# Performance work log

Hardware: AMD Instinct MI355X
Metric: run time of the kernel (lower is better)

Reference implementation:

```python
import math
import jax, jax.numpy as jnp
import numpy as np

B, S, D, H = 4, 1024, 512, 8
DH = D // H  # 64
SQRT_DIM = math.sqrt(D)


def _relative_shift(pos_score):
    # pos_score: [B, H, S, S]
    b, h, s1, s2 = pos_score.shape
    zeros = jnp.zeros((b, h, s1, 1), dtype=pos_score.dtype)
    padded = jnp.concatenate([zeros, pos_score], axis=-1)      # [B,H,S,S+1]
    padded = padded.reshape(b, h, s2 + 1, s1)                  # [B,H,S+1,S]
    return padded[:, :, 1:].reshape(b, h, s1, s2)


def setup_inputs() -> dict:
    key = jax.random.key(0)
    ks = jax.random.split(key, 14)
    std = 0.02
    inp = {
        "query": jax.random.normal(ks[0], (B, S, D), jnp.float32),
        "key": jax.random.normal(ks[1], (B, S, D), jnp.float32),
        "value": jax.random.normal(ks[2], (B, S, D), jnp.float32),
        "pos_embedding": jax.random.normal(ks[3], (B, S, D), jnp.float32),
        # projection weights stored [in, out] so y = x @ W + b
        "Wq": jax.random.normal(ks[4], (D, D), jnp.float32) * std,
        "bq": jnp.zeros((D,), jnp.float32),
        "Wk": jax.random.normal(ks[5], (D, D), jnp.float32) * std,
        "bk": jnp.zeros((D,), jnp.float32),
        "Wv": jax.random.normal(ks[6], (D, D), jnp.float32) * std,
        "bv": jnp.zeros((D,), jnp.float32),
        "Wp": jax.random.normal(ks[7], (D, D), jnp.float32) * std,  # pos_proj, no bias
        "Wo": jax.random.normal(ks[8], (D, D), jnp.float32) * std,
        "bo": jnp.zeros((D,), jnp.float32),
        "u_bias": jax.random.normal(ks[9], (H, DH), jnp.float32) * std,
        "v_bias": jax.random.normal(ks[10], (H, DH), jnp.float32) * std,
    }
    return inp


def reference(query, key, value, pos_embedding, Wq, bq, Wk, bk, Wv, bv, Wp, Wo, bo, u_bias, v_bias):
    b = query.shape[0]
    q = (query @ Wq + bq).reshape(b, -1, H, DH)          # [B,S,H,DH]
    k = (key @ Wk + bk).reshape(b, -1, H, DH)            # [B,T,H,DH]
    v = (value @ Wv + bv).reshape(b, -1, H, DH)          # [B,T,H,DH]
    p = (pos_embedding @ Wp).reshape(b, -1, H, DH)       # [B,T,H,DH]

    # content score: (q + u) . k  -> [B,H,S,T]
    content_score = jnp.einsum('bshd,bthd->bhst', q + u_bias, k)
    # position score: (q + v) . pos -> [B,H,S,T], then relative shift
    pos_score = jnp.einsum('bshd,bthd->bhst', q + v_bias, p)
    pos_score = _relative_shift(pos_score)

    score = (content_score + pos_score) / SQRT_DIM
    attn = jax.nn.softmax(score, axis=-1)                # dropout p=0 (eval)

    context = jnp.einsum('bhst,bthd->bshd', attn, v).reshape(b, -1, D)
    out = context @ Wo + bo
    return (out, attn)
```

## Files before the change

kernel.cpp:

```cpp
#include <hip/hip_runtime.h>

#define B_  4
#define S_  1024
#define D_  512
#define H_  8
#define DH_ 64
#define SCALE 0.044194173824159216f

typedef short bf16x8 __attribute__((ext_vector_type(8)));
typedef float f32x4  __attribute__((ext_vector_type(4)));

__device__ __forceinline__ unsigned short f2bf(float x) {
    union { float f; unsigned int u; } v; v.f = x;
    unsigned int r = v.u + 0x7fffu + ((v.u >> 16) & 1u);
    return (unsigned short)(r >> 16);
}
__device__ __forceinline__ float bf2f(unsigned short h) {
    union { unsigned int u; float f; } v; v.u = ((unsigned int)h) << 16;
    return v.f;
}

__global__ __launch_bounds__(256) void convert_wt_k(
    const float* __restrict__ W0, const float* __restrict__ W1,
    const float* __restrict__ W2, const float* __restrict__ W3,
    const float* __restrict__ W4,
    unsigned short* __restrict__ T0, unsigned short* __restrict__ T1,
    unsigned short* __restrict__ T2, unsigned short* __restrict__ T3,
    unsigned short* __restrict__ T4)
{
    const float* W;
    unsigned short* T;
    switch (blockIdx.y) {
        case 0: W = W0; T = T0; break;
        case 1: W = W1; T = T1; break;
        case 2: W = W2; T = T2; break;
        case 3: W = W3; T = T3; break;
        default: W = W4; T = T4; break;
    }
    const int e = blockIdx.x * 256 + threadIdx.x;
    const int o = e >> 9, i = e & 511;
    T[(size_t)o * 512 + i] = f2bf(W[(size_t)i * 512 + o]);
}

__global__ __launch_bounds__(256) void proj_all_k(
    const float* __restrict__ Aq_, const float* __restrict__ Ak_,
    const float* __restrict__ Ap_, const float* __restrict__ Av_,
    const unsigned short* __restrict__ WqT, const unsigned short* __restrict__ WkT,
    const unsigned short* __restrict__ WpT, const unsigned short* __restrict__ WvT,
    const float* __restrict__ bq, const float* __restrict__ bk,
    const float* __restrict__ bv,
    const float* __restrict__ ub, const float* __restrict__ vb,
    unsigned short* __restrict__ qu, unsigned short* __restrict__ qv,
    unsigned short* __restrict__ kbf, unsigned short* __restrict__ pbf,
    unsigned short* __restrict__ vT)
{
    __shared__ unsigned short Ab[64][72];
    __shared__ unsigned short Bb[64][72];
    const int mode = blockIdx.z;
    const float* A;
    const unsigned short* BT;
    switch (mode) {
        case 0: A = Aq_; BT = WqT; break;
        case 1: A = Ak_; BT = WkT; break;
        case 2: A = Ap_; BT = WpT; break;
        default: A = Av_; BT = WvT; break;
    }
    const int tid = threadIdx.x;
    const int i0 = blockIdx.x * 64, j0 = blockIdx.y * 64;
    const int w = tid >> 6, lane = tid & 63, l15 = lane & 15, lhi = lane >> 4;
    const int mr0 = (w >> 1) * 32, nc0 = (w & 1) * 32;
    f32x4 acc[2][2] = {};

    for (int k0 = 0; k0 < 512; k0 += 64) {
        __syncthreads();
#pragma unroll
        for (int it = 0; it < 4; ++it) {
            const int s = tid + it * 256;
            const int row = s >> 4, f4 = (s & 15) * 4;
            float4 va = *(const float4*)&A[(size_t)(i0 + row) * 512 + k0 + f4];
            ushort4 hh;
            hh.x = f2bf(va.x); hh.y = f2bf(va.y); hh.z = f2bf(va.z); hh.w = f2bf(va.w);
            *(ushort4*)&Ab[row][f4] = hh;
        }
#pragma unroll
        for (int it = 0; it < 2; ++it) {
            const int s = tid + it * 256;
            const int row = s >> 3, g = (s & 7) * 8;
            *(bf16x8*)&Bb[row][g] = *(const bf16x8*)&BT[(size_t)(j0 + row) * 512 + k0 + g];
        }
        __syncthreads();
#pragma unroll
        for (int kk = 0; kk < 2; ++kk) {
            bf16x8 a0 = *(const bf16x8*)&Ab[mr0 + l15][kk * 32 + lhi * 8];
            bf16x8 a1 = *(const bf16x8*)&Ab[mr0 + 16 + l15][kk * 32 + lhi * 8];
            bf16x8 b0 = *(const bf16x8*)&Bb[nc0 + l15][kk * 32 + lhi * 8];
            bf16x8 b1 = *(const bf16x8*)&Bb[nc0 + 16 + l15][kk * 32 + lhi * 8];
            acc[0][0] = __builtin_amdgcn_mfma_f32_16x16x32_bf16(a0, b0, acc[0][0], 0, 0, 0);
            acc[0][1] = __builtin_amdgcn_mfma_f32_16x16x32_bf16(a0, b1, acc[0][1], 0, 0, 0);
            acc[1][0] = __builtin_amdgcn_mfma_f32_16x16x32_bf16(a1, b0, acc[1][0], 0, 0, 0);
            acc[1][1] = __builtin_amdgcn_mfma_f32_16x16x32_bf16(a1, b1, acc[1][1], 0, 0, 0);
        }
    }

#pragma unroll
    for (int m = 0; m < 2; ++m)
#pragma unroll
        for (int n = 0; n < 2; ++n)
#pragma unroll
            for (int r = 0; r < 4; ++r) {
                const int grow = i0 + mr0 + 16 * m + 4 * lhi + r;
                const int gcol = j0 + nc0 + 16 * n + l15;
                const int b = grow >> 10, s = grow & 1023;
                const int h = gcol >> 6, d = gcol & 63;
                const float v = acc[m][n][r];
                if (mode == 3) {
                    const size_t idx = (((size_t)(b * H_ + h)) * DH_ + d) * S_ + s;
                    vT[idx] = f2bf(v + bv[gcol]);
                } else {
                    const size_t idx = (((size_t)b * H_ + h) * S_ + s) * DH_ + d;
                    if (mode == 0) {
                        const float base = v + bq[gcol];
                        qu[idx] = f2bf(base + ub[gcol]);
                        qv[idx] = f2bf(base + vb[gcol]);
                    } else if (mode == 1) {
                        kbf[idx] = f2bf(v + bk[gcol]);
                    } else {
                        pbf[idx] = f2bf(v);
                    }
                }
            }
}

__global__ __launch_bounds__(256) void gemm_bf16_k(
    const unsigned short* __restrict__ A,
    const unsigned short* __restrict__ BT,
    const float* __restrict__ bias,
    float* __restrict__ C)
{
    __shared__ unsigned short Ab[64][72];
    __shared__ unsigned short Bb[64][72];
    const int tid = threadIdx.x;
    const int i0 = blockIdx.x * 64, j0 = blockIdx.y * 64;
    const int w = tid >> 6, lane = tid & 63, l15 = lane & 15, lhi = lane >> 4;
    const int mr0 = (w >> 1) * 32, nc0 = (w & 1) * 32;
    f32x4 acc[2][2] = {};

    for (int k0 = 0; k0 < 512; k0 += 64) {
        __syncthreads();
#pragma unroll
        for (int it = 0; it < 2; ++it) {
            const int s = tid + it * 256;
            const int row = s >> 3, g = (s & 7) * 8;
            *(bf16x8*)&Ab[row][g] = *(const bf16x8*)&A[(size_t)(i0 + row) * 512 + k0 + g];
            *(bf16x8*)&Bb[row][g] = *(const bf16x8*)&BT[(size_t)(j0 + row) * 512 + k0 + g];
        }
        __syncthreads();
#pragma unroll
        for (int kk = 0; kk < 2; ++kk) {
            bf16x8 a0 = *(const bf16x8*)&Ab[mr0 + l15][kk * 32 + lhi * 8];
            bf16x8 a1 = *(const bf16x8*)&Ab[mr0 + 16 + l15][kk * 32 + lhi * 8];
            bf16x8 b0 = *(const bf16x8*)&Bb[nc0 + l15][kk * 32 + lhi * 8];
            bf16x8 b1 = *(const bf16x8*)&Bb[nc0 + 16 + l15][kk * 32 + lhi * 8];
            acc[0][0] = __builtin_amdgcn_mfma_f32_16x16x32_bf16(a0, b0, acc[0][0], 0, 0, 0);
            acc[0][1] = __builtin_amdgcn_mfma_f32_16x16x32_bf16(a0, b1, acc[0][1], 0, 0, 0);
            acc[1][0] = __builtin_amdgcn_mfma_f32_16x16x32_bf16(a1, b0, acc[1][0], 0, 0, 0);
            acc[1][1] = __builtin_amdgcn_mfma_f32_16x16x32_bf16(a1, b1, acc[1][1], 0, 0, 0);
        }
    }

#pragma unroll
    for (int m = 0; m < 2; ++m)
#pragma unroll
        for (int n = 0; n < 2; ++n)
#pragma unroll
            for (int r = 0; r < 4; ++r) {
                const int grow = i0 + mr0 + 16 * m + 4 * lhi + r;
                const int gcol = j0 + nc0 + 16 * n + l15;
                C[(size_t)grow * 512 + gcol] = acc[m][n][r] + bias[gcol];
            }
}

#define RS 1032
#define QBLK 16

__global__ __launch_bounds__(512, 4) void score_fused_k(
    const unsigned short* __restrict__ qu_g,
    const unsigned short* __restrict__ qv_g,
    const unsigned short* __restrict__ kb_g,
    const unsigned short* __restrict__ pb_g,
    const unsigned short* __restrict__ vT_g,
    float* __restrict__ attn,
    unsigned short* __restrict__ ctx_g)
{
    __shared__ unsigned short Qu[16][72];
    __shared__ unsigned short Aq[32][72];
    __shared__ unsigned short Kb[128][72];
    __shared__ unsigned short Pb[128][72];
    __shared__ unsigned short Rfl[17 * RS];
    __shared__ float red[16][9];

    const int tid = threadIdx.x;
    const int i0 = blockIdx.x * QBLK;
    const int bh = blockIdx.y;
    const int w = tid >> 6, lane = tid & 63, l15 = lane & 15, lhi = lane >> 4;

    const unsigned short* qu_b = qu_g + (size_t)bh * S_ * DH_;
    const unsigned short* qv_b = qv_g + (size_t)bh * S_ * DH_;
    const unsigned short* kb_b = kb_g + (size_t)bh * S_ * DH_;
    const unsigned short* pb_b = pb_g + (size_t)bh * S_ * DH_;

    if (tid < 128) {
        const int r = tid >> 3, seg = (tid & 7) * 8;
        *(bf16x8*)&Qu[r][seg] = *(const bf16x8*)&qu_b[(size_t)(i0 + r) * DH_ + seg];
    }
    if (tid < 256) {
        const int r = tid >> 3, seg = (tid & 7) * 8;
        const int src = min(i0 + r, S_ - 1);
        *(bf16x8*)&Aq[r][seg] = *(const bf16x8*)&qv_b[(size_t)src * DH_ + seg];
    }

    bf16x8 kreg[2], preg[2];
#pragma unroll
    for (int it = 0; it < 2; ++it) {
        const int s = tid + it * 512;
        const int row = s >> 3, seg = (s & 7) * 8;
        kreg[it] = *(const bf16x8*)&kb_b[(size_t)row * DH_ + seg];
        preg[it] = *(const bf16x8*)&pb_b[(size_t)row * DH_ + seg];
    }

    f32x4 acc[8] = {};
    for (int jc = 0; jc < 8; ++jc) {
        __syncthreads();
#pragma unroll
        for (int it = 0; it < 2; ++it) {
            const int s = tid + it * 512;
            const int row = s >> 3, seg = (s & 7) * 8;
            *(bf16x8*)&Kb[row][seg] = kreg[it];
            *(bf16x8*)&Pb[row][seg] = preg[it];
        }
        if (jc < 7) {
#pragma unroll
            for (int it = 0; it < 2; ++it) {
                const int s = tid + it * 512;
                const int row = (jc + 1) * 128 + (s >> 3), seg = (s & 7) * 8;
                kreg[it] = *(const bf16x8*)&kb_b[(size_t)row * DH_ + seg];
                preg[it] = *(const bf16x8*)&pb_b[(size_t)row * DH_ + seg];
            }
        }
        __syncthreads();

        f32x4 racc[2] = {};
#pragma unroll
        for (int kk = 0; kk < 2; ++kk) {
            bf16x8 pfr = *(const bf16x8*)&Pb[16 * w + l15][kk * 32 + lhi * 8];
            bf16x8 kfr = *(const bf16x8*)&Kb[16 * w + l15][kk * 32 + lhi * 8];
            bf16x8 aq0 = *(const bf16x8*)&Aq[l15][kk * 32 + lhi * 8];
            bf16x8 aq1 = *(const bf16x8*)&Aq[16 + l15][kk * 32 + lhi * 8];
            bf16x8 qf  = *(const bf16x8*)&Qu[l15][kk * 32 + lhi * 8];
            racc[0] = __builtin_amdgcn_mfma_f32_16x16x32_bf16(aq0, pfr, racc[0], 0, 0, 0);
            racc[1] = __builtin_amdgcn_mfma_f32_16x16x32_bf16(aq1, pfr, racc[1], 0, 0, 0);
            acc[jc] = __builtin_amdgcn_mfma_f32_16x16x32_bf16(qf,  kfr, acc[jc], 0, 0, 0);
        }
#pragma unroll
        for (int m = 0; m < 2; ++m)
#pragma unroll
            for (int r = 0; r < 4; ++r) {
                const int row = 16 * m + 4 * lhi + r;
                if (row < 17)
                    Rfl[row * RS + jc * 128 + 16 * w + l15] = f2bf(racc[m][r]);
            }
    }
    __syncthreads();

    const int il = 4 * lhi;
    float rmax[4], rsum[4];
#pragma unroll
    for (int r = 0; r < 4; ++r) rmax[r] = -3.0e38f;

#pragma unroll
    for (int jc = 0; jc < 8; ++jc)
#pragma unroll
        for (int r = 0; r < 4; ++r) {
            const int row = il + r;
            const int i = i0 + row;
            const int j = jc * 128 + 16 * w + l15;
            float pos = 0.f;
            if (j <= i)          pos = bf2f(Rfl[row * RS + 1023 - i + j]);
            else if (j >= i + 2) pos = bf2f(Rfl[(row + 1) * RS + (j - i - 2)]);
            const float s = (acc[jc][r] + pos) * SCALE;
            acc[jc][r] = s;
            rmax[r] = fmaxf(rmax[r], s);
        }

#pragma unroll
    for (int r = 0; r < 4; ++r)
#pragma unroll
        for (int off = 1; off < 16; off <<= 1)
            rmax[r] = fmaxf(rmax[r], __shfl_xor(rmax[r], off));
    if (l15 == 0)
#pragma unroll
        for (int r = 0; r < 4; ++r) red[il + r][w] = rmax[r];
    __syncthreads();
#pragma unroll
    for (int r = 0; r < 4; ++r) {
        float mx = red[il + r][0];
#pragma unroll
        for (int ww = 1; ww < 8; ++ww) mx = fmaxf(mx, red[il + r][ww]);
        rmax[r] = mx;
        rsum[r] = 0.f;
    }
    __syncthreads();

#pragma unroll
    for (int jc = 0; jc < 8; ++jc)
#pragma unroll
        for (int r = 0; r < 4; ++r) {
            const float e = __expf(acc[jc][r] - rmax[r]);
            acc[jc][r] = e;
            rsum[r] += e;
        }
#pragma unroll
    for (int r = 0; r < 4; ++r)
#pragma unroll
        for (int off = 1; off < 16; off <<= 1)
            rsum[r] += __shfl_xor(rsum[r], off);
    if (l15 == 0)
#pragma unroll
        for (int r = 0; r < 4; ++r) red[il + r][w] = rsum[r];
    __syncthreads();

    float* attn_b = attn + (size_t)bh * S_ * S_;
#pragma unroll
    for (int r = 0; r < 4; ++r) {
        float sum = red[il + r][0];
#pragma unroll
        for (int ww = 1; ww < 8; ++ww) sum += red[il + r][ww];
        const float inv = 1.f / sum;
#pragma unroll
        for (int jc = 0; jc < 8; ++jc) {
            const int j = jc * 128 + 16 * w + l15;
            const float pn = acc[jc][r] * inv;
            attn_b[(size_t)(i0 + il + r) * S_ + j] = pn;
            Rfl[(il + r) * RS + j] = f2bf(pn);
        }
    }
    __syncthreads();

    const int b4 = bh >> 3, h4 = bh & 7;
    const int nblk = w & 3;
    const int kh = w >> 2;
    const unsigned short* vrow = vT_g + (size_t)bh * DH_ * S_
                               + (size_t)(16 * nblk + l15) * S_;
    f32x4 cacc = {};
#pragma unroll
    for (int ki = 0; ki < 16; ++ki) {
        const int t0 = kh * 512 + ki * 32 + lhi * 8;
        bf16x8 a  = *(const bf16x8*)&Rfl[l15 * RS + t0];
        bf16x8 bb = *(const bf16x8*)&vrow[t0];
        cacc = __builtin_amdgcn_mfma_f32_16x16x32_bf16(a, bb, cacc, 0, 0, 0);
    }
    float* fred = (float*)&Kb[0][0];
    if (kh == 0) {
#pragma unroll
        for (int r = 0; r < 4; ++r)
            fred[(nblk * 16 + 4 * lhi + r) * 16 + l15] = cacc[r];
    }
    __syncthreads();
    if (kh == 1) {
#pragma unroll
        for (int r = 0; r < 4; ++r) {
            const float vs = cacc[r] + fred[(nblk * 16 + 4 * lhi + r) * 16 + l15];
            const int srow = i0 + 4 * lhi + r;
            ctx_g[((size_t)(b4 * S_ + srow)) * D_ + h4 * DH_ + 16 * nblk + l15] = f2bf(vs);
        }
    }
}

extern "C" void kernel_launch(void* const* d_in, const int* in_sizes, int n_in,
                              void* d_out, int out_size, void* d_ws, size_t ws_size,
                              hipStream_t stream)
{
    const float* query = (const float*)d_in[0];
    const float* key_  = (const float*)d_in[1];
    const float* value = (const float*)d_in[2];
    const float* pose  = (const float*)d_in[3];
    const float* Wq = (const float*)d_in[4];
    const float* bq = (const float*)d_in[5];
    const float* Wk = (const float*)d_in[6];
    const float* bk = (const float*)d_in[7];
    const float* Wv = (const float*)d_in[8];
    const float* bv = (const float*)d_in[9];
    const float* Wp = (const float*)d_in[10];
    const float* Wo = (const float*)d_in[11];
    const float* bo = (const float*)d_in[12];
    const float* u_bias = (const float*)d_in[13];
    const float* v_bias = (const float*)d_in[14];

    const size_t NTOK = (size_t)B_ * S_ * D_;
    float* out  = (float*)d_out;
    float* attn = (float*)d_out + NTOK;

    unsigned short* qu  = (unsigned short*)d_ws;
    unsigned short* qv  = qu + NTOK;
    unsigned short* kbf = qv + NTOK;
    unsigned short* pbf = kbf + NTOK;
    unsigned short* WqT = pbf + NTOK;
    unsigned short* WkT = WqT + 262144;
    unsigned short* WpT = WkT + 262144;
    unsigned short* WvT = WpT + 262144;
    unsigned short* WoT = WvT + 262144;
    unsigned short* vT  = WoT + 262144;
    unsigned short* ctx = vT + NTOK;

    const dim3 blk256(256);
    const dim3 gproj(64, 8);

    convert_wt_k<<<dim3(1024, 5), blk256, 0, stream>>>(Wq, Wk, Wp, Wv, Wo,
                                                       WqT, WkT, WpT, WvT, WoT);

    proj_all_k<<<dim3(64, 8, 4), blk256, 0, stream>>>(
        query, key_, pose, value,
        WqT, WkT, WpT, WvT,
        bq, bk, bv, u_bias, v_bias,
        qu, qv, kbf, pbf, vT);

    score_fused_k<<<dim3(S_ / QBLK, B_ * H_), dim3(512), 0, stream>>>(
        qu, qv, kbf, pbf, vT, attn, ctx);

    gemm_bf16_k<<<gproj, blk256, 0, stream>>>(ctx, WoT, bo, out);
}
```

Baseline: 138.0 us.

## Load score operands straight to registers and tile the weight transpose through LDS

The fused score kernel no longer stages K and P chunks and the query tiles through shared memory with double barriers. Each wave now loads its MFMA fragments directly from global memory into registers, which removes the per-chunk __syncthreads pairs and cuts LDS use, so more blocks can fit per CU. The weight-transpose kernel now goes through a padded 64x64 LDS tile so both the reads and the writes are coalesced. The trade-off is that each row fragment is fetched from global memory by every block rather than once into shared memory, and the loads are no longer prefetched ahead of the MFMAs.

```diff
diff --git a/kernel.cpp b/kernel.cpp
--- a/kernel.cpp
+++ b/kernel.cpp
@@ -28,18 +28,25 @@
     unsigned short* __restrict__ T2, unsigned short* __restrict__ T3,
     unsigned short* __restrict__ T4)
 {
+    __shared__ float tile[64][65];
     const float* W;
     unsigned short* T;
-    switch (blockIdx.y) {
+    switch (blockIdx.z) {
         case 0: W = W0; T = T0; break;
         case 1: W = W1; T = T1; break;
         case 2: W = W2; T = T2; break;
         case 3: W = W3; T = T3; break;
         default: W = W4; T = T4; break;
     }
-    const int e = blockIdx.x * 256 + threadIdx.x;
-    const int o = e >> 9, i = e & 511;
-    T[(size_t)o * 512 + i] = f2bf(W[(size_t)i * 512 + o]);
+    const int r0 = blockIdx.y * 64, c0 = blockIdx.x * 64;
+    const int tx = threadIdx.x & 63, ty = threadIdx.x >> 6;
+#pragma unroll
+    for (int it = 0; it < 16; ++it)
+        tile[ty + 4 * it][tx] = W[(size_t)(r0 + ty + 4 * it) * 512 + c0 + tx];
+    __syncthreads();
+#pragma unroll
+    for (int it = 0; it < 16; ++it)
+        T[(size_t)(c0 + ty + 4 * it) * 512 + r0 + tx] = f2bf(tile[tx][ty + 4 * it]);
 }
 
 __global__ __launch_bounds__(256) void proj_all_k(
@@ -192,12 +199,9 @@
     float* __restrict__ attn,
     unsigned short* __restrict__ ctx_g)
 {
-    __shared__ unsigned short Qu[16][72];
-    __shared__ unsigned short Aq[32][72];
-    __shared__ unsigned short Kb[128][72];
-    __shared__ unsigned short Pb[128][72];
     __shared__ unsigned short Rfl[17 * RS];
     __shared__ float red[16][9];
+    __shared__ float fred[1024];
 
     const int tid = threadIdx.x;
     const int i0 = blockIdx.x * QBLK;
@@ -209,66 +213,45 @@
     const unsigned short* kb_b = kb_g + (size_t)bh * S_ * DH_;
     const unsigned short* pb_b = pb_g + (size_t)bh * S_ * DH_;
 
-    if (tid < 128) {
-        const int r = tid >> 3, seg = (tid & 7) * 8;
-        *(bf16x8*)&Qu[r][seg] = *(const bf16x8*)&qu_b[(size_t)(i0 + r) * DH_ + seg];
-    }
-    if (tid < 256) {
-        const int r = tid >> 3, seg = (tid & 7) * 8;
-        const int src = min(i0 + r, S_ - 1);
-        *(bf16x8*)&Aq[r][seg] = *(const bf16x8*)&qv_b[(size_t)src * DH_ + seg];
-    }
-
-    bf16x8 kreg[2], preg[2];
-#pragma unroll
-    for (int it = 0; it < 2; ++it) {
-        const int s = tid + it * 512;
-        const int row = s >> 3, seg = (s & 7) * 8;
-        kreg[it] = *(const bf16x8*)&kb_b[(size_t)row * DH_ + seg];
-        preg[it] = *(const bf16x8*)&pb_b[(size_t)row * DH_ + seg];
+    bf16x8 qf[2], aq0[2], aq1[2];
+    {
+        const int qrow  = i0 + l15;
+        const int qrow1 = min(i0 + 16 + l15, S_ - 1);
+#pragma unroll
+        for (int kk = 0; kk < 2; ++kk) {
+            const int off = kk * 32 + lhi * 8;
+            qf[kk]  = *(const bf16x8*)&qu_b[(size_t)qrow  * DH_ + off];
+            aq0[kk] = *(const bf16x8*)&qv_b[(size_t)qrow  * DH_ + off];
+            aq1[kk] = *(const bf16x8*)&qv_b[(size_t)qrow1 * DH_ + off];
+        }
     }
 
     f32x4 acc[8] = {};
+#pragma unroll
     for (int jc = 0; jc < 8; ++jc) {
-        __syncthreads();
-#pragma unroll
-        for (int it = 0; it < 2; ++it) {
-            const int s = tid + it * 512;
-            const int row = s >> 3, seg = (s & 7) * 8;
-            *(bf16x8*)&Kb[row][seg] = kreg[it];
-            *(bf16x8*)&Pb[row][seg] = preg[it];
-        }
-        if (jc < 7) {
-#pragma unroll
-            for (int it = 0; it < 2; ++it) {
-                const int s = tid + it * 512;
-                const int row = (jc + 1) * 128 + (s >> 3), seg = (s & 7) * 8;
-                kreg[it] = *(const bf16x8*)&kb_b[(size_t)row * DH_ + seg];
-                preg[it] = *(const bf16x8*)&pb_b[(size_t)row * DH_ + seg];
-            }
-        }
-        __syncthreads();
-
-        f32x4 racc[2] = {};
-#pragma unroll
-        for (int kk = 0; kk < 2; ++kk) {
-            bf16x8 pfr = *(const bf16x8*)&Pb[16 * w + l15][kk * 32 + lhi * 8];
-            bf16x8 kfr = *(const bf16x8*)&Kb[16 * w + l15][kk * 32 + lhi * 8];
-            bf16x8 aq0 = *(const bf16x8*)&Aq[l15][kk * 32 + lhi * 8];
-            bf16x8 aq1 = *(const bf16x8*)&Aq[16 + l15][kk * 32 + lhi * 8];
-            bf16x8 qf  = *(const bf16x8*)&Qu[l15][kk * 32 + lhi * 8];
-            racc[0] = __builtin_amdgcn_mfma_f32_16x16x32_bf16(aq0, pfr, racc[0], 0, 0, 0);
-            racc[1] = __builtin_amdgcn_mfma_f32_16x16x32_bf16(aq1, pfr, racc[1], 0, 0, 0);
-            acc[jc] = __builtin_amdgcn_mfma_f32_16x16x32_bf16(qf,  kfr, acc[jc], 0, 0, 0);
-        }
-#pragma unroll
-        for (int m = 0; m < 2; ++m)
-#pragma unroll
-            for (int r = 0; r < 4; ++r) {
-                const int row = 16 * m + 4 * lhi + r;
-                if (row < 17)
-                    Rfl[row * RS + jc * 128 + 16 * w + l15] = f2bf(racc[m][r]);
-            }
+        const size_t krow = (size_t)(jc * 128 + 16 * w + l15) * DH_;
+        bf16x8 kfr0 = *(const bf16x8*)&kb_b[krow + lhi * 8];
+        bf16x8 kfr1 = *(const bf16x8*)&kb_b[krow + 32 + lhi * 8];
+        bf16x8 pfr0 = *(const bf16x8*)&pb_b[krow + lhi * 8];
+        bf16x8 pfr1 = *(const bf16x8*)&pb_b[krow + 32 + lhi * 8];
+
+        f32x4 racc0 = {}, racc1 = {};
+        racc0 = __builtin_amdgcn_mfma_f32_16x16x32_bf16(aq0[0], pfr0, racc0, 0, 0, 0);
+        racc0 = __builtin_amdgcn_mfma_f32_16x16x32_bf16(aq0[1], pfr1, racc0, 0, 0, 0);
+        racc1 = __builtin_amdgcn_mfma_f32_16x16x32_bf16(aq1[0], pfr0, racc1, 0, 0, 0);
+        racc1 = __builtin_amdgcn_mfma_f32_16x16x32_bf16(aq1[1], pfr1, racc1, 0, 0, 0);
+        acc[jc] = __builtin_amdgcn_mfma_f32_16x16x32_bf16(qf[0], kfr0, acc[jc], 0, 0, 0);
+        acc[jc] = __builtin_amdgcn_mfma_f32_16x16x32_bf16(qf[1], kfr1, acc[jc], 0, 0, 0);
+
+        const int col = jc * 128 + 16 * w + l15;
+#pragma unroll
+        for (int r = 0; r < 4; ++r) {
+            const int row0 = 4 * lhi + r;
+            Rfl[row0 * RS + col] = f2bf(racc0[r]);
+            const int row1 = 16 + 4 * lhi + r;
+            if (row1 < 17)
+                Rfl[row1 * RS + col] = f2bf(racc1[r]);
+        }
     }
     __syncthreads();
 
@@ -359,7 +342,6 @@
         bf16x8 bb = *(const bf16x8*)&vrow[t0];
         cacc = __builtin_amdgcn_mfma_f32_16x16x32_bf16(a, bb, cacc, 0, 0, 0);
     }
-    float* fred = (float*)&Kb[0][0];
     if (kh == 0) {
 #pragma unroll
         for (int r = 0; r < 4; ++r)
@@ -415,7 +397,7 @@
     const dim3 blk256(256);
     const dim3 gproj(64, 8);
 
-    convert_wt_k<<<dim3(1024, 5), blk256, 0, stream>>>(Wq, Wk, Wp, Wv, Wo,
+    convert_wt_k<<<dim3(8, 8, 5), blk256, 0, stream>>>(Wq, Wk, Wp, Wv, Wo,
                                                        WqT, WkT, WpT, WvT, WoT);
 
     proj_all_k<<<dim3(64, 8, 4), blk256, 0, stream>>>(
```

Result: slower. 158.3 us (+14.7%).
